# Performance work log

Measured on AMD Instinct MI355X. Metric: run time of the kernel, lower is better.

The kernel has to match this reference:

```python
import jax, jax.numpy as jnp
import numpy as np

IN_C, OUT_C, K, STRIDE, PAD = 128, 256, 3, 1, 1
B, H, W = 32, 56, 56


def setup_inputs() -> dict:
    key = jax.random.key(0)
    kx, kw = jax.random.split(key)
    x = jax.random.normal(kx, (B, IN_C, H, W), dtype=jnp.float32)
    # He init, matching torch.randn(out_c,in_c,k,k) * (2/(in_c*k*k))**0.5
    Wk = jax.random.normal(kw, (OUT_C, IN_C, K, K), dtype=jnp.float32) * (2.0 / (IN_C * K * K)) ** 0.5
    b = jnp.zeros((OUT_C,), dtype=jnp.float32)
    return {"x": x, "Wk": Wk, "b": b}


def reference(x, Wk, b):
    # Same math as the module's zero-pad + im2col + GEMM pipeline,
    # expressed as a direct convolution (implicit GEMM).
    out = jax.lax.conv_general_dilated(
        x, Wk,
        window_strides=(STRIDE, STRIDE),
        padding=[(PAD, PAD), (PAD, PAD)],
        dimension_numbers=("NCHW", "OIHW", "NCHW"),
    )
    return out + b[None, :, None, None]
```

## Files before the change

### kernel.cpp

```cpp
#include <hip/hip_runtime.h>
#include <hip/hip_bf16.h>

#define IN_C  128
#define OUT_C 256
#define HIMG  56
#define WIMG  56
#define BIMG  32
#define HW    (HIMG * WIMG)
#define KW    1152

#define BM    128
#define TH    4
#define XROWS 6
#define XCOLS 58
#define NPIXT (XROWS * XCOLS)

typedef __attribute__((ext_vector_type(8))) short short8;
typedef __attribute__((ext_vector_type(4))) float float4_;

__device__ __forceinline__ unsigned short f32_to_bf16_rne(float f) {
    unsigned u = __builtin_bit_cast(unsigned, f);
    u += 0x7FFFu + ((u >> 16) & 1u);
    return (unsigned short)(u >> 16);
}

__global__ void repack_w(const float* __restrict__ Wk, unsigned short* __restrict__ Wt) {
    int idx = blockIdx.x * 256 + threadIdx.x;
    if (idx >= OUT_C * KW) return;
    int oc  = idx / KW;
    int rem = idx - oc * KW;
    int r   = rem >> 7;
    int ic  = rem & 127;
    Wt[idx] = f32_to_bf16_rne(Wk[oc * KW + ic * 9 + r]);
}

__global__ __launch_bounds__(256, 2) void conv_gemm(
    const float* __restrict__ x, const unsigned short* __restrict__ Wt,
    const float* __restrict__ bias, float* __restrict__ out)
{
    __shared__ short Xs[NPIXT * 32];

    const int tid  = threadIdx.x;
    const int lane = tid & 63;
    const int wid  = tid >> 6;
    const int bx   = blockIdx.x;
    const int b    = bx / 14;
    const int h0   = (bx - b * 14) * TH;
    const int oc0  = blockIdx.y * BM;

    const int wm = (wid >> 1) * 64;
    const int wn = (wid & 1) * 112;

    int lp0[7], outoff[7];
    #pragma unroll
    for (int ni = 0; ni < 7; ++ni) {
        int nl  = wn + ni * 16 + (lane & 15);
        int ht_ = nl / 56;
        int wt_ = nl - ht_ * 56;
        lp0[ni]    = (ht_ + 1) * XCOLS + (wt_ + 1);
        outoff[ni] = (h0 + ht_) * WIMG + wt_;
    }

    const unsigned short* aLane = Wt + (size_t)(oc0 + wm + (lane & 15)) * KW + (lane >> 4) * 8;

    float4_ acc[4][7];
    #pragma unroll
    for (int mi = 0; mi < 4; ++mi)
        #pragma unroll
        for (int ni = 0; ni < 7; ++ni) acc[mi][ni] = (float4_)0.0f;

    const int q = lane >> 4;

    short8 anx[4];
    #pragma unroll
    for (int mi = 0; mi < 4; ++mi)
        anx[mi] = *(const short8*)(aLane + (size_t)mi * 16 * KW);

    for (int t = 0; t < 36; ++t) {
        const int icq = t / 9;
        const int r   = t - icq * 9;

        if (r == 0) {
            if (t) __syncthreads();
            for (int pix = tid; pix < NPIXT; pix += 256) {
                int row  = pix / XCOLS;
                int colw = pix - row * XCOLS;
                int h = h0 + row - 1;
                int w = colw - 1;
                bool valid = ((unsigned)h < HIMG) & ((unsigned)w < WIMG);
                const int sw = (pix >> 1) & 3;
                #pragma unroll
                for (int qb = 0; qb < 4; ++qb) {
                    const float* src = x + (size_t)(b * IN_C + icq * 32 + qb * 8) * HW
                                         + (ptrdiff_t)(h * WIMG + w);
                    short8 v;
                    #pragma unroll
                    for (int j = 0; j < 8; ++j) {
                        float f = valid ? src[(size_t)j * HW] : 0.0f;
                        v[j] = (short)f32_to_bf16_rne(f);
                    }
                    *(short8*)&Xs[pix * 32 + (qb ^ sw) * 8] = v;
                }
            }
            __syncthreads();
        }

        short8 afr[4];
        #pragma unroll
        for (int mi = 0; mi < 4; ++mi) afr[mi] = anx[mi];
        if (t < 35) {
            const int t1   = t + 1;
            const int icq1 = t1 / 9;
            const int r1   = t1 - icq1 * 9;
            const int koff = r1 * 128 + icq1 * 32;
            #pragma unroll
            for (int mi = 0; mi < 4; ++mi)
                anx[mi] = *(const short8*)(aLane + (size_t)mi * 16 * KW + koff);
        }

        const int doff = (r / 3 - 1) * XCOLS + (r - (r / 3) * 3 - 1);
        short8 bfr[7];
        #pragma unroll
        for (int ni = 0; ni < 7; ++ni) {
            int lp   = lp0[ni] + doff;
            int slot = q ^ ((lp >> 1) & 3);
            bfr[ni]  = *(const short8*)&Xs[lp * 32 + slot * 8];
        }
        #pragma unroll
        for (int mi = 0; mi < 4; ++mi)
            #pragma unroll
            for (int ni = 0; ni < 7; ++ni)
                acc[mi][ni] = __builtin_amdgcn_mfma_f32_16x16x32_bf16(
                    afr[mi], bfr[ni], acc[mi][ni], 0, 0, 0);
    }

    const int rowg = (lane >> 4) * 4;
    #pragma unroll
    for (int mi = 0; mi < 4; ++mi) {
        #pragma unroll
        for (int v = 0; v < 4; ++v) {
            const int oc = oc0 + wm + mi * 16 + rowg + v;
            const float bv = bias[oc];
            float* obase = out + (size_t)(b * OUT_C + oc) * HW;
            #pragma unroll
            for (int ni = 0; ni < 7; ++ni)
                obase[outoff[ni]] = acc[mi][ni][v] + bv;
        }
    }
}

extern "C" void kernel_launch(void* const* d_in, const int* in_sizes, int n_in,
                              void* d_out, int out_size, void* d_ws, size_t ws_size,
                              hipStream_t stream) {
    const float* x    = (const float*)d_in[0];
    const float* Wk   = (const float*)d_in[1];
    const float* bias = (const float*)d_in[2];
    float* out        = (float*)d_out;
    unsigned short* Wt = (unsigned short*)d_ws;

    repack_w<<<dim3((OUT_C * KW + 255) / 256), dim3(256), 0, stream>>>(Wk, Wt);
    conv_gemm<<<dim3(BIMG * (HIMG / TH), OUT_C / BM), dim3(256), 0, stream>>>(x, Wt, bias, out);
}
```

Baseline: 229.3 us.

## Pre-convert input to NHWC bf16 and fragment-order weights for conv GEMM

New measurement: 220.2 us. -4.0%, faster.

```diff
diff --git a/kernel.cpp b/kernel.cpp
--- a/kernel.cpp
+++ b/kernel.cpp
@@ -14,6 +14,7 @@
 #define XROWS 6
 #define XCOLS 58
 #define NPIXT (XROWS * XCOLS)
+#define NFRAG (36 * 16)
 
 typedef __attribute__((ext_vector_type(8))) short short8;
 typedef __attribute__((ext_vector_type(4))) float float4_;
@@ -24,18 +25,40 @@
     return (unsigned short)(u >> 16);
 }
 
-__global__ void repack_w(const float* __restrict__ Wk, unsigned short* __restrict__ Wt) {
+__global__ void prep_w2(const float* __restrict__ Wk, unsigned short* __restrict__ Wt2) {
     int idx = blockIdx.x * 256 + threadIdx.x;
-    if (idx >= OUT_C * KW) return;
-    int oc  = idx / KW;
-    int rem = idx - oc * KW;
-    int r   = rem >> 7;
-    int ic  = rem & 127;
-    Wt[idx] = f32_to_bf16_rne(Wk[oc * KW + ic * 9 + r]);
-}
-
+    if (idx >= NFRAG * 64) return;
+    int lane = idx & 63;
+    int fg   = idx >> 6;
+    int g    = fg & 15, t = fg >> 4;
+    int icq  = t / 9, r = t - icq * 9;
+    int oc   = g * 16 + (lane & 15);
+    int icb  = icq * 32 + (lane >> 4) * 8;
+    short8 v;
+    #pragma unroll
+    for (int jj = 0; jj < 8; ++jj)
+        v[jj] = (short)f32_to_bf16_rne(Wk[(size_t)oc * KW + (icb + jj) * 9 + r]);
+    *(short8*)(Wt2 + (size_t)idx * 8) = v;
+}
+
+__global__ void prep_x(const float* __restrict__ x, unsigned short* __restrict__ xp) {
+    int idx = blockIdx.x * 256 + threadIdx.x;
+    int c8  = idx & 15;
+    int pix = idx >> 4;
+    int b   = pix / HW;
+    int hw  = pix - b * HW;
+    const float* src = x + (size_t)(b * IN_C + c8 * 8) * HW + hw;
+    short8 v;
+    #pragma unroll
+    for (int j = 0; j < 8; ++j)
+        v[j] = (short)f32_to_bf16_rne(src[(size_t)j * HW]);
+    *(short8*)(xp + (size_t)pix * IN_C + c8 * 8) = v;
+}
+
+template<bool XP>
 __global__ __launch_bounds__(256, 2) void conv_gemm(
-    const float* __restrict__ x, const unsigned short* __restrict__ Wt,
+    const float* __restrict__ x, const unsigned short* __restrict__ xp,
+    const unsigned short* __restrict__ Wt2,
     const float* __restrict__ bias, float* __restrict__ out)
 {
     __shared__ short Xs[NPIXT * 32];
@@ -48,20 +71,17 @@
     const int h0   = (bx - b * 14) * TH;
     const int oc0  = blockIdx.y * BM;
 
-    const int wm = (wid >> 1) * 64;
-    const int wn = (wid & 1) * 112;
-
-    int lp0[7], outoff[7];
-    #pragma unroll
-    for (int ni = 0; ni < 7; ++ni) {
-        int nl  = wn + ni * 16 + (lane & 15);
-        int ht_ = nl / 56;
-        int wt_ = nl - ht_ * 56;
-        lp0[ni]    = (ht_ + 1) * XCOLS + (wt_ + 1);
-        outoff[ni] = (h0 + ht_) * WIMG + wt_;
-    }
-
-    const unsigned short* aLane = Wt + (size_t)(oc0 + wm + (lane & 15)) * KW + (lane >> 4) * 8;
+    const int wm   = (wid >> 1) * 64;
+    const int wrow = (wid & 1) * 2;
+    const int j    = lane & 15;
+    const int q    = lane >> 4;
+
+    const int hloc = wrow + (j >> 3);
+    const int lp00 = (hloc + 1) * XCOLS + (j & 7) + 1;
+    const int out0 = (h0 + hloc) * WIMG + (j & 7);
+
+    const unsigned short* aPtr =
+        Wt2 + ((size_t)((oc0 >> 4) + (wm >> 4)) * 64 + lane) * 8;
 
     float4_ acc[4][7];
     #pragma unroll
@@ -69,12 +89,10 @@
         #pragma unroll
         for (int ni = 0; ni < 7; ++ni) acc[mi][ni] = (float4_)0.0f;
 
-    const int q = lane >> 4;
-
     short8 anx[4];
     #pragma unroll
     for (int mi = 0; mi < 4; ++mi)
-        anx[mi] = *(const short8*)(aLane + (size_t)mi * 16 * KW);
+        anx[mi] = *(const short8*)(aPtr + mi * 512);
 
     for (int t = 0; t < 36; ++t) {
         const int icq = t / 9;
@@ -82,24 +100,40 @@
 
         if (r == 0) {
             if (t) __syncthreads();
-            for (int pix = tid; pix < NPIXT; pix += 256) {
-                int row  = pix / XCOLS;
-                int colw = pix - row * XCOLS;
-                int h = h0 + row - 1;
-                int w = colw - 1;
-                bool valid = ((unsigned)h < HIMG) & ((unsigned)w < WIMG);
-                const int sw = (pix >> 1) & 3;
-                #pragma unroll
-                for (int qb = 0; qb < 4; ++qb) {
-                    const float* src = x + (size_t)(b * IN_C + icq * 32 + qb * 8) * HW
-                                         + (ptrdiff_t)(h * WIMG + w);
-                    short8 v;
+            if (XP) {
+                const unsigned short* xpb =
+                    xp + (size_t)b * HW * IN_C + icq * 32;
+                for (int c = tid; c < NPIXT * 4; c += 256) {
+                    int p = c >> 2, qb = c & 3;
+                    int row  = p / XCOLS;
+                    int colw = p - row * XCOLS;
+                    int h = h0 + row - 1, w = colw - 1;
+                    bool valid = ((unsigned)h < HIMG) & ((unsigned)w < WIMG);
+                    short8 v = (short8)0;
+                    if (valid)
+                        v = *(const short8*)(xpb + (size_t)(h * WIMG + w) * IN_C + qb * 8);
+                    int sw = (p >> 1) & 3;
+                    *(short8*)&Xs[p * 32 + ((qb ^ sw) * 8)] = v;
+                }
+            } else {
+                for (int p = tid; p < NPIXT; p += 256) {
+                    int row  = p / XCOLS;
+                    int colw = p - row * XCOLS;
+                    int h = h0 + row - 1, w = colw - 1;
+                    bool valid = ((unsigned)h < HIMG) & ((unsigned)w < WIMG);
+                    int sw = (p >> 1) & 3;
                     #pragma unroll
-                    for (int j = 0; j < 8; ++j) {
-                        float f = valid ? src[(size_t)j * HW] : 0.0f;
-                        v[j] = (short)f32_to_bf16_rne(f);
+                    for (int qb = 0; qb < 4; ++qb) {
+                        const float* src = x + (size_t)(b * IN_C + icq * 32 + qb * 8) * HW
+                                             + (ptrdiff_t)(h * WIMG + w);
+                        short8 v;
+                        #pragma unroll
+                        for (int jj = 0; jj < 8; ++jj) {
+                            float f = valid ? src[(size_t)jj * HW] : 0.0f;
+                            v[jj] = (short)f32_to_bf16_rne(f);
+                        }
+                        *(short8*)&Xs[p * 32 + ((qb ^ sw) * 8)] = v;
                     }
-                    *(short8*)&Xs[pix * 32 + (qb ^ sw) * 8] = v;
                 }
             }
             __syncthreads();
@@ -109,23 +143,21 @@
         #pragma unroll
         for (int mi = 0; mi < 4; ++mi) afr[mi] = anx[mi];
         if (t < 35) {
-            const int t1   = t + 1;
-            const int icq1 = t1 / 9;
-            const int r1   = t1 - icq1 * 9;
-            const int koff = r1 * 128 + icq1 * 32;
+            const unsigned short* aNxt = aPtr + (size_t)(t + 1) * 16 * 512;
             #pragma unroll
             for (int mi = 0; mi < 4; ++mi)
-                anx[mi] = *(const short8*)(aLane + (size_t)mi * 16 * KW + koff);
+                anx[mi] = *(const short8*)(aNxt + mi * 512);
         }
 
         const int doff = (r / 3 - 1) * XCOLS + (r - (r / 3) * 3 - 1);
+        const int lpb  = lp00 + doff;
+        const int slot = q ^ ((lpb >> 1) & 3);
+        const short* bbase = &Xs[lpb * 32 + slot * 8];
         short8 bfr[7];
         #pragma unroll
-        for (int ni = 0; ni < 7; ++ni) {
-            int lp   = lp0[ni] + doff;
-            int slot = q ^ ((lp >> 1) & 3);
-            bfr[ni]  = *(const short8*)&Xs[lp * 32 + slot * 8];
-        }
+        for (int ni = 0; ni < 7; ++ni)
+            bfr[ni] = *(const short8*)(bbase + ni * 256);
+
         #pragma unroll
         for (int mi = 0; mi < 4; ++mi)
             #pragma unroll
@@ -141,10 +173,10 @@
         for (int v = 0; v < 4; ++v) {
             const int oc = oc0 + wm + mi * 16 + rowg + v;
             const float bv = bias[oc];
-            float* obase = out + (size_t)(b * OUT_C + oc) * HW;
+            float* obase = out + (size_t)(b * OUT_C + oc) * HW + out0;
             #pragma unroll
             for (int ni = 0; ni < 7; ++ni)
-                obase[outoff[ni]] = acc[mi][ni][v] + bv;
+                obase[ni * 8] = acc[mi][ni][v] + bv;
         }
     }
 }
@@ -156,8 +188,20 @@
     const float* Wk   = (const float*)d_in[1];
     const float* bias = (const float*)d_in[2];
     float* out        = (float*)d_out;
-    unsigned short* Wt = (unsigned short*)d_ws;
-
-    repack_w<<<dim3((OUT_C * KW + 255) / 256), dim3(256), 0, stream>>>(Wk, Wt);
-    conv_gemm<<<dim3(BIMG * (HIMG / TH), OUT_C / BM), dim3(256), 0, stream>>>(x, Wt, bias, out);
-}
+
+    unsigned short* Wt2 = (unsigned short*)d_ws;
+    const size_t xp_off   = (size_t)NFRAG * 64 * 8 * 2;
+    const size_t xp_bytes = (size_t)BIMG * HW * IN_C * 2;
+    unsigned short* xp = (unsigned short*)((char*)d_ws + xp_off);
+    const bool use_xp = ws_size >= xp_off + xp_bytes;
+
+    prep_w2<<<dim3((NFRAG * 64 + 255) / 256), dim3(256), 0, stream>>>(Wk, Wt2);
+    if (use_xp) {
+        prep_x<<<dim3(BIMG * HW * 16 / 256), dim3(256), 0, stream>>>(x, xp);
+        conv_gemm<true><<<dim3(BIMG * (HIMG / TH), OUT_C / BM), dim3(256), 0, stream>>>(
+            x, xp, Wt2, bias, out);
+    } else {
+        conv_gemm<false><<<dim3(BIMG * (HIMG / TH), OUT_C / BM), dim3(256), 0, stream>>>(
+            x, xp, Wt2, bias, out);
+    }
+}
```
